# Kernel optimization log

Hardware: AMD Instinct MI355X
Metric: run time of the kernel (lower is better)

## Reference

```python
import jax, jax.numpy as jnp
import numpy as np

NUM_HEADS = 8


def conv2x2_s2(x, w, b):
    # x: [B,C,H,W], w: [O,I,2,2], stride 2, no padding (torch Conv2d k=2,s=2)
    y = jax.lax.conv_general_dilated(
        x, w, window_strides=(2, 2), padding='VALID',
        dimension_numbers=('NCHW', 'OIHW', 'NCHW'))
    return y + b[None, :, None, None]


def up2(x):
    return jnp.repeat(jnp.repeat(x, 2, axis=2), 2, axis=3)


def setup_inputs() -> dict:
    key = jax.random.key(0)
    B, C, H, W = 1, 128, 64, 64
    N = H * W
    ks = jax.random.split(key, 7)
    p = lambda k, shape: jax.random.normal(k, shape, jnp.float32) * 0.02
    return {
        'x': jax.random.normal(ks[0], (B, N, C), jnp.float32),
        'conv1_w': p(ks[1], (C, C, 2, 2)),
        'conv1_b': jnp.zeros((C,), jnp.float32),
        'conv2_w': p(ks[2], (C, C, 2, 2)),
        'conv2_b': jnp.zeros((C,), jnp.float32),
        'q_w': p(ks[3], (C, C)),
        'kv_w': p(ks[4], (2 * C, C)),
        'proj_w': p(ks[5], (C, C)),
        'proj_b': jnp.zeros((C,), jnp.float32),
        'H': H,
        'W': W,
    }


def reference(x, conv1_w, conv1_b, conv2_w, conv2_b, q_w, kv_w, proj_w, proj_b, H, W):
    B, N, C = x.shape
    hd = C // NUM_HEADS
    scale = hd ** -0.5
    # tokens -> feature map
    x_ = x.transpose(0, 2, 1).reshape(B, C, H, W)
    # ChannelPriorQueries: conv(s2) -> up2 -> conv(s2) -> up2 (HxW preserved)
    tq = up2(conv2x2_s2(up2(conv2x2_s2(x_, conv1_w, conv1_b)), conv2_w, conv2_b))
    tq = tq.reshape(B, C, N).transpose(0, 2, 1)  # [B,N,C]
    # projections (torch Linear: y = x @ W.T)
    q = (tq @ q_w.T).reshape(B, N, NUM_HEADS, hd).transpose(0, 2, 1, 3)   # [B,h,N,d]
    kv = (x @ kv_w.T).reshape(B, N, 2, NUM_HEADS, hd).transpose(2, 0, 3, 1, 4)
    k, v = kv[0], kv[1]  # [B,h,N,d]
    # sr_ratio == 1: F.interpolate(q, size=(N, d)) is the identity
    attn = jax.nn.softmax(jnp.einsum('bhqd,bhkd->bhqk', q, k) * scale, axis=-1)
    out = jnp.einsum('bhqk,bhkd->bhqd', attn, v)
    out = out.transpose(0, 2, 1, 3).reshape(B, N, C)
    return out @ proj_w.T + proj_b
```

## Files before the change

kernel.cpp:

```cpp
#include <hip/hip_runtime.h>
#include <hip/hip_bf16.h>

#define CCH 128
#define NTOK 4096
#define NP 1024
#define NH 8
#define HD 16

typedef __attribute__((ext_vector_type(8)))  short s8v;
typedef __attribute__((ext_vector_type(16))) float f32x16;

#define OFF_Y1T   0
#define OFF_M     131072
#define OFF_QB    147456
#define OFF_AT16  147584
#define OFF_K16   180352
#define OFF_VT16  442496
#define OFF_Q16   704640

__device__ inline unsigned short f2bf(float v) {
    __hip_bfloat16 b = __float2bfloat16(v);
    return *reinterpret_cast<unsigned short*>(&b);
}
__device__ inline unsigned int pk2bf(float a, float b) {
    __hip_bfloat162 t = __float22bfloat162_rn(make_float2(a, b));
    return *reinterpret_cast<unsigned int*>(&t);
}
__device__ inline int crow_of(int r, int hi) { return (r & 3) + 8*(r >> 2) + 4*hi; }

union BU { unsigned int u[4]; s8v v; };

__global__ void __launch_bounds__(256) kA_prep(const float* __restrict__ x,
        const float* __restrict__ w1, const float* __restrict__ b1,
        const float* __restrict__ w2, const float* __restrict__ b2,
        const float* __restrict__ qw, const float* __restrict__ kvw,
        float* __restrict__ ws,
        unsigned short* __restrict__ k16, unsigned short* __restrict__ vt16) {
    __shared__ float smem[2048];
    const int b = blockIdx.x;
    const int tid = threadIdx.x;
    const int w = tid >> 6, lane = tid & 63;
    const int ql = lane & 31, hi = lane >> 5;

    if (b < 256) {
        const int n0 = (b >> 1) * 32;
        const int octile = (b & 1) * 4 + w;
        const int oc0 = octile * 32;
        const bool isK = (octile < 4);
        const float* arow = (isK ? x + (n0 + ql)*CCH : kvw + (oc0 + ql)*CCH) + hi*8;
        const float* brow = (isK ? kvw + (oc0 + ql)*CCH : x + (n0 + ql)*CCH) + hi*8;
        f32x16 acc = {};
        float4 a0 = *reinterpret_cast<const float4*>(arow);
        float4 a1 = *reinterpret_cast<const float4*>(arow + 4);
        float4 b0 = *reinterpret_cast<const float4*>(brow);
        float4 b1v = *reinterpret_cast<const float4*>(brow + 4);
        for (int kk = 0; kk < 8; ++kk) {
            float4 na0 = a0, na1 = a1, nb0 = b0, nb1 = b1v;
            if (kk < 7) {
                na0 = *reinterpret_cast<const float4*>(arow + (kk+1)*16);
                na1 = *reinterpret_cast<const float4*>(arow + (kk+1)*16 + 4);
                nb0 = *reinterpret_cast<const float4*>(brow + (kk+1)*16);
                nb1 = *reinterpret_cast<const float4*>(brow + (kk+1)*16 + 4);
            }
            BU au, bu;
            au.u[0] = pk2bf(a0.x, a0.y); au.u[1] = pk2bf(a0.z, a0.w);
            au.u[2] = pk2bf(a1.x, a1.y); au.u[3] = pk2bf(a1.z, a1.w);
            bu.u[0] = pk2bf(b0.x, b0.y); bu.u[1] = pk2bf(b0.z, b0.w);
            bu.u[2] = pk2bf(b1v.x, b1v.y); bu.u[3] = pk2bf(b1v.z, b1v.w);
            acc = __builtin_amdgcn_mfma_f32_32x32x16_bf16(au.v, bu.v, acc, 0, 0, 0);
            a0 = na0; a1 = na1; b0 = nb0; b1v = nb1;
        }
        if (isK) {
            const int oc = oc0 + ql, h = oc >> 4, d = oc & 15;
            #pragma unroll
            for (int r = 0; r < 16; ++r) {
                const int n = n0 + crow_of(r, hi);
                k16[(h*NTOK + n)*HD + d] = f2bf(acc[r]);
            }
        } else {
            #pragma unroll
            for (int r = 0; r < 16; ++r) {
                const int oc = oc0 + crow_of(r, hi);
                vt16[(oc - CCH)*NTOK + n0 + ql] = f2bf(acc[r]);
            }
        }
    } else if (b < 512) {
        const int pp = tid >> 7, o = tid & 127;
        float* xs = smem + pp * 1024;
        const int p0 = (b - 256) * 4 + pp * 2;
        #pragma unroll
        for (int pl = 0; pl < 2; ++pl) {
            int p = p0 + pl;
            int i = p >> 5, j = p & 31;
            int t00 = (2*i)*64 + 2*j;
            float4 v;
            v.x = x[(t00     )*CCH + o];
            v.y = x[(t00 +  1)*CCH + o];
            v.z = x[(t00 + 64)*CCH + o];
            v.w = x[(t00 + 65)*CCH + o];
            *reinterpret_cast<float4*>(&xs[(pl*CCH + o)*4]) = v;
        }
        __syncthreads();
        float acc0 = 0.f, acc1 = 0.f;
        #pragma unroll 8
        for (int c = 0; c < CCH; ++c) {
            float4 w4 = *reinterpret_cast<const float4*>(&w1[(o*CCH + c)*4]);
            float4 a  = *reinterpret_cast<const float4*>(&xs[c*4]);
            float4 bq = *reinterpret_cast<const float4*>(&xs[(CCH + c)*4]);
            acc0 += w4.x*a.x + w4.y*a.y + w4.z*a.z + w4.w*a.w;
            acc1 += w4.x*bq.x + w4.y*bq.y + w4.z*bq.z + w4.w*bq.w;
        }
        ws[OFF_Y1T + (p0+0)*CCH + o] = acc0 + b1[o];
        ws[OFF_Y1T + (p0+1)*CCH + o] = acc1 + b1[o];
    } else {
        int id = (b - 512) * 256 + tid;
        int r = id >> 7, c = id & 127;
        const float* qr = qw + r*CCH;
        float acc = 0.f;
        #pragma unroll 4
        for (int o4 = 0; o4 < 32; ++o4) {
            float4 q4 = *reinterpret_cast<const float4*>(qr + o4*4);
            float4 wa = *reinterpret_cast<const float4*>(&w2[((o4*4+0)*CCH + c)*4]);
            float4 wb = *reinterpret_cast<const float4*>(&w2[((o4*4+1)*CCH + c)*4]);
            float4 wc = *reinterpret_cast<const float4*>(&w2[((o4*4+2)*CCH + c)*4]);
            float4 wd = *reinterpret_cast<const float4*>(&w2[((o4*4+3)*CCH + c)*4]);
            acc += q4.x*(wa.x+wa.y+wa.z+wa.w);
            acc += q4.y*(wb.x+wb.y+wb.z+wb.w);
            acc += q4.z*(wc.x+wc.y+wc.z+wc.w);
            acc += q4.w*(wd.x+wd.y+wd.z+wd.w);
        }
        ws[OFF_M + id] = acc * 0.25f;
        if (id < CCH) {
            float a = 0.f;
            #pragma unroll 8
            for (int o = 0; o < CCH; ++o) a += qw[id*CCH + o] * b2[o];
            ws[OFF_QB + id] = a * 0.25f;
        }
    }
}

__global__ void __launch_bounds__(256) kQ_qproj(const float* __restrict__ ws,
                                                unsigned short* __restrict__ q16) {
    const int id = blockIdx.x * 256 + threadIdx.x;
    const int d = id & 15, p = (id >> 4) & 1023, h = id >> 14;
    const float* Mr = ws + OFF_M + (h*HD + d)*CCH;
    const float* yr = ws + OFF_Y1T + p*CCH;
    float a = 0.f;
    #pragma unroll 8
    for (int c4 = 0; c4 < 32; ++c4) {
        float4 m4 = *reinterpret_cast<const float4*>(Mr + c4*4);
        float4 y4 = *reinterpret_cast<const float4*>(yr + c4*4);
        a += m4.x*y4.x + m4.y*y4.y + m4.z*y4.z + m4.w*y4.w;
    }
    q16[id] = f2bf(a + ws[OFF_QB + h*HD + d]);
}

__global__ void __launch_bounds__(1024) kB_attn(const unsigned short* __restrict__ q16,
                                                const unsigned short* __restrict__ k16,
                                                const unsigned short* __restrict__ vt16,
                                                unsigned short* __restrict__ at16) {
    __shared__ float oacc[16*HD*32];
    __shared__ float lbuf[16*32];
    const int tid = threadIdx.x;
    const int h = blockIdx.x & 7, qt = blockIdx.x >> 3;
    const int s = tid >> 6;
    const int lane = tid & 63;
    const int ql = lane & 31;
    const int hi = lane >> 5;

    s8v qf = *reinterpret_cast<const s8v*>(q16 + (h*NP + qt*32 + ql)*HD + hi*8);

    const unsigned short* kp = k16 + (h*NTOK)*HD;
    const unsigned short* vp = vt16 + (h*HD + ql)*NTOK;
    const bool vvalid = (ql < HD);

    f32x16 acc = {};
    float lsum = 0.f;

    const int kbase = s*256;
    s8v kf = *reinterpret_cast<const s8v*>(kp + (kbase + ql)*HD + hi*8);
    s8v vf1 = {}, vf2 = {};
    if (vvalid) {
        vf1 = *reinterpret_cast<const s8v*>(vp + kbase + hi*8);
        vf2 = *reinterpret_cast<const s8v*>(vp + kbase + 16 + hi*8);
    }

    for (int c = 0; c < 8; ++c) {
        s8v kf_n = kf, vf1_n = vf1, vf2_n = vf2;
        if (c < 7) {
            const int kb2 = kbase + (c+1)*32;
            kf_n = *reinterpret_cast<const s8v*>(kp + (kb2 + ql)*HD + hi*8);
            if (vvalid) {
                vf1_n = *reinterpret_cast<const s8v*>(vp + kb2 + hi*8);
                vf2_n = *reinterpret_cast<const s8v*>(vp + kb2 + 16 + hi*8);
            }
        }

        f32x16 z = {};
        f32x16 st = __builtin_amdgcn_mfma_f32_32x32x16_bf16(kf, qf, z, 0, 0, 0);

        float p[16];
        #pragma unroll
        for (int r = 0; r < 16; ++r) p[r] = __expf(st[r]);
        float t0 = (p[0]+p[1]) + (p[2]+p[3]);
        float t1 = (p[4]+p[5]) + (p[6]+p[7]);
        float t2 = (p[8]+p[9]) + (p[10]+p[11]);
        float t3 = (p[12]+p[13]) + (p[14]+p[15]);
        lsum += (t0 + t1) + (t2 + t3);

        unsigned int W[8];
        #pragma unroll
        for (int i = 0; i < 8; ++i) W[i] = pk2bf(p[2*i], p[2*i+1]);

        BU b1x, b2x;
        {
            unsigned int s0 = (unsigned int)__shfl_xor((int)W[0], 32);
            unsigned int s1 = (unsigned int)__shfl_xor((int)W[1], 32);
            unsigned int s2 = (unsigned int)__shfl_xor((int)W[2], 32);
            unsigned int s3 = (unsigned int)__shfl_xor((int)W[3], 32);
            b1x.u[0] = hi ? s2 : W[0];
            b1x.u[1] = hi ? s3 : W[1];
            b1x.u[2] = hi ? W[2] : s0;
            b1x.u[3] = hi ? W[3] : s1;
            unsigned int s4 = (unsigned int)__shfl_xor((int)W[4], 32);
            unsigned int s5 = (unsigned int)__shfl_xor((int)W[5], 32);
            unsigned int s6 = (unsigned int)__shfl_xor((int)W[6], 32);
            unsigned int s7 = (unsigned int)__shfl_xor((int)W[7], 32);
            b2x.u[0] = hi ? s6 : W[4];
            b2x.u[1] = hi ? s7 : W[5];
            b2x.u[2] = hi ? W[6] : s4;
            b2x.u[3] = hi ? W[7] : s5;
        }

        acc = __builtin_amdgcn_mfma_f32_32x32x16_bf16(vf1, b1x.v, acc, 0, 0, 0);
        acc = __builtin_amdgcn_mfma_f32_32x32x16_bf16(vf2, b2x.v, acc, 0, 0, 0);

        kf = kf_n; vf1 = vf1_n; vf2 = vf2_n;
    }

    float lt = lsum + __shfl_xor(lsum, 32);
    if (lane < 32) lbuf[s*32 + ql] = lt;
    #pragma unroll
    for (int r = 0; r < 8; ++r) {
        int d = crow_of(r, hi);
        oacc[(s*HD + d)*32 + ql] = acc[r];
    }
    __syncthreads();

    if (tid < 512) {
        const int q2 = tid & 31, d2 = tid >> 5;
        float ltot = 0.f, o = 0.f;
        #pragma unroll
        for (int ss = 0; ss < 16; ++ss) {
            ltot += lbuf[ss*32 + q2];
            o    += oacc[(ss*HD + d2)*32 + q2];
        }
        at16[(qt*32 + q2)*CCH + h*HD + d2] = f2bf(o / ltot);
    }
}

__global__ void __launch_bounds__(256) k5_proj(const unsigned short* __restrict__ at16,
                                               const float* __restrict__ pw,
                                               const float* __restrict__ pb,
                                               float* __restrict__ out) {
    const int ptile = blockIdx.x;
    const int w = threadIdx.x >> 6, lane = threadIdx.x & 63;
    const int ql = lane & 31, hi = lane >> 5;
    const int oc0 = w * 32;
    const unsigned short* arow = at16 + (ptile*32 + ql)*CCH + hi*8;
    const float* brow = pw + (oc0 + ql)*CCH + hi*8;

    f32x16 acc = {};
    s8v af = *reinterpret_cast<const s8v*>(arow);
    float4 b0 = *reinterpret_cast<const float4*>(brow);
    float4 b1v = *reinterpret_cast<const float4*>(brow + 4);
    for (int kk = 0; kk < 8; ++kk) {
        s8v naf = af; float4 nb0 = b0, nb1 = b1v;
        if (kk < 7) {
            naf = *reinterpret_cast<const s8v*>(arow + (kk+1)*16);
            nb0 = *reinterpret_cast<const float4*>(brow + (kk+1)*16);
            nb1 = *reinterpret_cast<const float4*>(brow + (kk+1)*16 + 4);
        }
        BU bu;
        bu.u[0] = pk2bf(b0.x, b0.y); bu.u[1] = pk2bf(b0.z, b0.w);
        bu.u[2] = pk2bf(b1v.x, b1v.y); bu.u[3] = pk2bf(b1v.z, b1v.w);
        acc = __builtin_amdgcn_mfma_f32_32x32x16_bf16(af, bu.v, acc, 0, 0, 0);
        af = naf; b0 = nb0; b1v = nb1;
    }

    const float bias = pb[oc0 + ql];
    #pragma unroll
    for (int r = 0; r < 16; ++r) {
        const int j = crow_of(r, hi);
        const int t00 = 128*ptile + 2*j;
        const float v = acc[r] + bias;
        out[(t00     )*CCH + oc0 + ql] = v;
        out[(t00 +  1)*CCH + oc0 + ql] = v;
        out[(t00 + 64)*CCH + oc0 + ql] = v;
        out[(t00 + 65)*CCH + oc0 + ql] = v;
    }
}

extern "C" void kernel_launch(void* const* d_in, const int* in_sizes, int n_in,
                              void* d_out, int out_size, void* d_ws, size_t ws_size,
                              hipStream_t stream) {
    const float* x   = (const float*)d_in[0];
    const float* w1  = (const float*)d_in[1];
    const float* b1  = (const float*)d_in[2];
    const float* w2  = (const float*)d_in[3];
    const float* b2  = (const float*)d_in[4];
    const float* qw  = (const float*)d_in[5];
    const float* kvw = (const float*)d_in[6];
    const float* pw  = (const float*)d_in[7];
    const float* pb  = (const float*)d_in[8];
    float* ws  = (float*)d_ws;
    float* out = (float*)d_out;

    unsigned short* at16 = (unsigned short*)(ws + OFF_AT16);
    unsigned short* k16  = (unsigned short*)(ws + OFF_K16);
    unsigned short* vt16 = (unsigned short*)(ws + OFF_VT16);
    unsigned short* q16  = (unsigned short*)(ws + OFF_Q16);

    hipLaunchKernelGGL(kA_prep, dim3(576), dim3(256), 0, stream,
                       x, w1, b1, w2, b2, qw, kvw, ws, k16, vt16);
    hipLaunchKernelGGL(kQ_qproj, dim3(512), dim3(256), 0, stream, ws, q16);
    hipLaunchKernelGGL(kB_attn, dim3(256), dim3(1024), 0, stream,
                       q16, k16, vt16, at16);
    hipLaunchKernelGGL(k5_proj, dim3(32), dim3(256), 0, stream, at16, pw, pb, out);
}
```

Before: 55.96 us.

## Split attention key range across two blocks and combine partials in projection

The attention kernel now splits the 4096 keys into two halves handled by separate blocks, doubling the grid from 256 to 512 blocks of 1024 threads. Each block writes unnormalized fp32 partial outputs and row sums to workspace. The projection kernel adds the two partials, normalizes, and converts to bf16 before the MFMA. This aims to fill more compute units in the attention stage. The cost is extra fp32 partial traffic and the loss of software prefetching in the projection loop.

```diff
diff --git a/kernel.cpp b/kernel.cpp
--- a/kernel.cpp
+++ b/kernel.cpp
@@ -13,10 +13,11 @@
 #define OFF_Y1T   0
 #define OFF_M     131072
 #define OFF_QB    147456
-#define OFF_AT16  147584
-#define OFF_K16   180352
-#define OFF_VT16  442496
-#define OFF_Q16   704640
+#define OFF_Q16   147584
+#define OFF_K16   213120
+#define OFF_VT16  475264
+#define OFF_ATP   737408
+#define OFF_LP    999552
 
 __device__ inline unsigned short f2bf(float v) {
     __hip_bfloat16 b = __float2bfloat16(v);
@@ -158,11 +159,12 @@
 __global__ void __launch_bounds__(1024) kB_attn(const unsigned short* __restrict__ q16,
                                                 const unsigned short* __restrict__ k16,
                                                 const unsigned short* __restrict__ vt16,
-                                                unsigned short* __restrict__ at16) {
+                                                float* __restrict__ atp,
+                                                float* __restrict__ lp) {
     __shared__ float oacc[16*HD*32];
     __shared__ float lbuf[16*32];
     const int tid = threadIdx.x;
-    const int h = blockIdx.x & 7, qt = blockIdx.x >> 3;
+    const int h = blockIdx.x & 7, qt = (blockIdx.x >> 3) & 31, kh = blockIdx.x >> 8;
     const int s = tid >> 6;
     const int lane = tid & 63;
     const int ql = lane & 31;
@@ -177,7 +179,7 @@
     f32x16 acc = {};
     float lsum = 0.f;
 
-    const int kbase = s*256;
+    const int kbase = kh*2048 + s*128;
     s8v kf = *reinterpret_cast<const s8v*>(kp + (kbase + ql)*HD + hi*8);
     s8v vf1 = {}, vf2 = {};
     if (vvalid) {
@@ -185,9 +187,9 @@
         vf2 = *reinterpret_cast<const s8v*>(vp + kbase + 16 + hi*8);
     }
 
-    for (int c = 0; c < 8; ++c) {
+    for (int c = 0; c < 4; ++c) {
         s8v kf_n = kf, vf1_n = vf1, vf2_n = vf2;
-        if (c < 7) {
+        if (c < 3) {
             const int kb2 = kbase + (c+1)*32;
             kf_n = *reinterpret_cast<const s8v*>(kp + (kb2 + ql)*HD + hi*8);
             if (vvalid) {
@@ -255,11 +257,14 @@
             ltot += lbuf[ss*32 + q2];
             o    += oacc[(ss*HD + d2)*32 + q2];
         }
-        at16[(qt*32 + q2)*CCH + h*HD + d2] = f2bf(o / ltot);
-    }
-}
-
-__global__ void __launch_bounds__(256) k5_proj(const unsigned short* __restrict__ at16,
+        const int p = qt*32 + q2;
+        atp[kh*(NP*CCH) + p*CCH + h*HD + d2] = o;
+        if (d2 == 0) lp[kh*(NP*NH) + p*NH + h] = ltot;
+    }
+}
+
+__global__ void __launch_bounds__(256) k5_proj(const float* __restrict__ atp,
+                                               const float* __restrict__ lp,
                                                const float* __restrict__ pw,
                                                const float* __restrict__ pb,
                                                float* __restrict__ out) {
@@ -267,25 +272,30 @@
     const int w = threadIdx.x >> 6, lane = threadIdx.x & 63;
     const int ql = lane & 31, hi = lane >> 5;
     const int oc0 = w * 32;
-    const unsigned short* arow = at16 + (ptile*32 + ql)*CCH + hi*8;
+    const int p = ptile*32 + ql;
     const float* brow = pw + (oc0 + ql)*CCH + hi*8;
 
     f32x16 acc = {};
-    s8v af = *reinterpret_cast<const s8v*>(arow);
-    float4 b0 = *reinterpret_cast<const float4*>(brow);
-    float4 b1v = *reinterpret_cast<const float4*>(brow + 4);
     for (int kk = 0; kk < 8; ++kk) {
-        s8v naf = af; float4 nb0 = b0, nb1 = b1v;
-        if (kk < 7) {
-            naf = *reinterpret_cast<const s8v*>(arow + (kk+1)*16);
-            nb0 = *reinterpret_cast<const float4*>(brow + (kk+1)*16);
-            nb1 = *reinterpret_cast<const float4*>(brow + (kk+1)*16 + 4);
-        }
+        const float l = lp[p*NH + kk] + lp[NP*NH + p*NH + kk];
+        const float rl = 1.f / l;
+        const int base = p*CCH + kk*16 + hi*8;
+        float4 a0 = *reinterpret_cast<const float4*>(atp + base);
+        float4 a1 = *reinterpret_cast<const float4*>(atp + base + 4);
+        float4 c0 = *reinterpret_cast<const float4*>(atp + NP*CCH + base);
+        float4 c1 = *reinterpret_cast<const float4*>(atp + NP*CCH + base + 4);
+        BU af;
+        af.u[0] = pk2bf((a0.x+c0.x)*rl, (a0.y+c0.y)*rl);
+        af.u[1] = pk2bf((a0.z+c0.z)*rl, (a0.w+c0.w)*rl);
+        af.u[2] = pk2bf((a1.x+c1.x)*rl, (a1.y+c1.y)*rl);
+        af.u[3] = pk2bf((a1.z+c1.z)*rl, (a1.w+c1.w)*rl);
+
+        float4 b0 = *reinterpret_cast<const float4*>(brow + kk*16);
+        float4 b1v = *reinterpret_cast<const float4*>(brow + kk*16 + 4);
         BU bu;
         bu.u[0] = pk2bf(b0.x, b0.y); bu.u[1] = pk2bf(b0.z, b0.w);
         bu.u[2] = pk2bf(b1v.x, b1v.y); bu.u[3] = pk2bf(b1v.z, b1v.w);
-        acc = __builtin_amdgcn_mfma_f32_32x32x16_bf16(af, bu.v, acc, 0, 0, 0);
-        af = naf; b0 = nb0; b1v = nb1;
+        acc = __builtin_amdgcn_mfma_f32_32x32x16_bf16(af.v, bu.v, acc, 0, 0, 0);
     }
 
     const float bias = pb[oc0 + ql];
@@ -316,15 +326,17 @@
     float* ws  = (float*)d_ws;
     float* out = (float*)d_out;
 
-    unsigned short* at16 = (unsigned short*)(ws + OFF_AT16);
+    unsigned short* q16  = (unsigned short*)(ws + OFF_Q16);
     unsigned short* k16  = (unsigned short*)(ws + OFF_K16);
     unsigned short* vt16 = (unsigned short*)(ws + OFF_VT16);
-    unsigned short* q16  = (unsigned short*)(ws + OFF_Q16);
+    float* atp = ws + OFF_ATP;
+    float* lp  = ws + OFF_LP;
 
     hipLaunchKernelGGL(kA_prep, dim3(576), dim3(256), 0, stream,
                        x, w1, b1, w2, b2, qw, kvw, ws, k16, vt16);
     hipLaunchKernelGGL(kQ_qproj, dim3(512), dim3(256), 0, stream, ws, q16);
-    hipLaunchKernelGGL(kB_attn, dim3(256), dim3(1024), 0, stream,
-                       q16, k16, vt16, at16);
-    hipLaunchKernelGGL(k5_proj, dim3(32), dim3(256), 0, stream, at16, pw, pb, out);
-}
+    hipLaunchKernelGGL(kB_attn, dim3(512), dim3(1024), 0, stream,
+                       q16, k16, vt16, atp, lp);
+    hipLaunchKernelGGL(k5_proj, dim3(32), dim3(256), 0, stream,
+                       atp, lp, pw, pb, out);
+}
```

New measurement: 63.20 us. 12.9% more time.
